# Optimization experiments

Measured on AMD Instinct MI355X. Metric: run time of the kernel, lower is better.

The kernel has to match this reference:

```python
import jax, jax.numpy as jnp
import numpy as np

N_NODES = 100000
N_EDGES = 1600000
D_IN = 256
D_OUT = 128


def setup_inputs() -> dict:
    key = jax.random.key(0)
    ks = jax.random.split(key, 7)
    h = jax.random.normal(ks[0], (N_NODES, D_IN), dtype=jnp.float32)
    src = jax.random.randint(ks[1], (N_EDGES,), 0, N_NODES, dtype=jnp.int32)
    dst = jax.random.randint(ks[2], (N_EDGES,), 0, N_NODES, dtype=jnp.int32)
    W = jax.random.normal(ks[3], (D_IN, D_OUT), dtype=jnp.float32) * (1.0 / np.sqrt(D_IN))
    b = jax.random.normal(ks[4], (D_OUT,), dtype=jnp.float32) * 0.01
    w_att = jax.random.normal(ks[5], (2 * D_OUT, 1), dtype=jnp.float32) * (1.0 / np.sqrt(2 * D_OUT))
    b_att = jax.random.normal(ks[6], (1,), dtype=jnp.float32) * 0.01
    return {"h": h, "src": src, "dst": dst, "W": W, "b": b, "w_att": w_att, "b_att": b_att}


def reference(h, src, dst, W, b, w_att, b_att):
    # node projection: graph.ndata['h'] = self.linear(h)
    hp = h @ W + b  # [N, D_OUT]
    n = hp.shape[0]
    d = hp.shape[1]
    # edge attention: leaky_relu(att_linear(cat[h_src, h_dst]))
    # cat([hs, hd]) @ w_att == hs @ w_att[:d] + hd @ w_att[d:]  (avoids [E, 2d] concat)
    wa_s = w_att[:d, 0]  # [D_OUT]
    wa_d = w_att[d:, 0]  # [D_OUT]
    e = hp[src] @ wa_s + hp[dst] @ wa_d + b_att[0]  # [E]
    e = jax.nn.leaky_relu(e)  # default negative_slope 0.01 matches F.leaky_relu
    # segment softmax over each destination node's incoming edges
    emax = jax.ops.segment_max(e, dst, num_segments=n)  # [N]
    ex = jnp.exp(e - emax[dst])  # [E]
    denom = jax.ops.segment_sum(ex, dst, num_segments=n)  # [N]
    # weighted scatter-sum of src features: sum_e alpha_e * h_src_e
    num = jax.ops.segment_sum(ex[:, None] * hp[src], dst, num_segments=n)  # [N, D_OUT]
    out = num / jnp.where(denom > 0, denom, 1.0)[:, None]  # zero-in-degree nodes -> 0
    return out
```

## Files before the change

### kernel.cpp

```cpp
#include <hip/hip_runtime.h>
#include <hip/hip_bf16.h>

#define D_IN 256
#define D_OUT 128
#define BNODES 64
#define BCAP 1536
#define EPB 8192
#define MAXNB 1600

typedef __attribute__((ext_vector_type(8))) short bf16x8;
typedef __attribute__((ext_vector_type(4))) float f32x4;
typedef __attribute__((ext_vector_type(2))) float f32x2;

__device__ __forceinline__ unsigned short f2bf(float f) {
    unsigned u = __float_as_uint(f);
    unsigned r = ((u >> 16) & 1u) + 0x7FFFu;
    return (unsigned short)((u + r) >> 16);
}
__device__ __forceinline__ unsigned pk2(float a, float b) {
    return (unsigned)f2bf(a) | ((unsigned)f2bf(b) << 16);
}
__device__ __forceinline__ bf16x8 pack8(float4 a, float4 b) {
    union { uint4 u; bf16x8 v; } r;
    r.u.x = pk2(a.x, a.y); r.u.y = pk2(a.z, a.w);
    r.u.z = pk2(b.x, b.y); r.u.w = pk2(b.z, b.w);
    return r.v;
}
__device__ __forceinline__ void gload_lds16(const void* g, void* l) {
    __builtin_amdgcn_global_load_lds(
        (const __attribute__((address_space(1))) void*)g,
        (__attribute__((address_space(3))) void*)l, 16, 0, 0);
}

__global__ __launch_bounds__(256) void init_bcursor_kernel(int* __restrict__ bcursor, int nb)
{
    int i = blockIdx.x * 256 + threadIdx.x;
    if (i < nb) bcursor[i] = i * BCAP;
}

__global__ __launch_bounds__(256) void prep_kernel(
    const float* __restrict__ W, unsigned short* __restrict__ WbT)
{
    int idx = blockIdx.x * 256 + threadIdx.x;
    int k = idx >> 7;
    int c = idx & 127;
    WbT[(size_t)c * 256 + k] = f2bf(W[idx]);
}

__global__ __launch_bounds__(512, 4) void gemm_mfma_kernel(
    const float* __restrict__ h, const unsigned short* __restrict__ WbT,
    const float* __restrict__ b, const float* __restrict__ w_att,
    unsigned short* __restrict__ hpb,
    float* __restrict__ alpha_s, float* __restrict__ alpha_d,
    int n, int nstrips)
{
    __shared__ char bT[65536];
    const int t = threadIdx.x;
    const int wv = t >> 6, lane = t & 63;
    const int fr = lane & 15, fq = lane >> 4;
    const int swz = (fr & 7) << 4;

    #pragma unroll
    for (int j = 0; j < 8; ++j) {
        int col0 = wv * 16 + j * 2;
        int col  = col0 + (lane >> 5);
        int seg  = lane & 31;
        const char* src = (const char*)WbT + col * 512 + ((seg * 16) ^ ((col & 7) << 4));
        gload_lds16(src, bT + col0 * 512);
    }
    __syncthreads();

    const int strip = blockIdx.x * 8 + wv;
    if (strip >= nstrips) return;
    const int r0 = strip * 32;

    const float* arow[2];
    #pragma unroll
    for (int m = 0; m < 2; ++m) {
        int rg = r0 + m * 16 + fr;
        if (rg >= n) rg = n - 1;
        arow[m] = h + (size_t)rg * D_IN + fq * 8;
    }

    f32x4 acc[2][8];
    #pragma unroll
    for (int m = 0; m < 2; ++m)
        #pragma unroll
        for (int nn = 0; nn < 8; ++nn) acc[m][nn] = (f32x4){0.f, 0.f, 0.f, 0.f};

    float4 bufA[2][2][2];
    #pragma unroll
    for (int m = 0; m < 2; ++m) {
        const float4* ap = (const float4*)arow[m];
        bufA[0][m][0] = ap[0]; bufA[0][m][1] = ap[1];
    }

    #pragma unroll
    for (int kk = 0; kk < 8; ++kk) {
        const int cur = kk & 1, nxt = cur ^ 1;
        if (kk < 7) {
            #pragma unroll
            for (int m = 0; m < 2; ++m) {
                const float4* ap = (const float4*)(arow[m] + (kk + 1) * 32);
                bufA[nxt][m][0] = ap[0]; bufA[nxt][m][1] = ap[1];
            }
        }
        bf16x8 af[2];
        #pragma unroll
        for (int m = 0; m < 2; ++m)
            af[m] = pack8(bufA[cur][m][0], bufA[cur][m][1]);

        const int x = kk * 64 + fq * 16;
        #pragma unroll
        for (int nn = 0; nn < 8; ++nn) {
            bf16x8 bfr = *(const bf16x8*)(bT + (nn * 16 + fr) * 512 + (x ^ swz));
            acc[0][nn] = __builtin_amdgcn_mfma_f32_16x16x32_bf16(af[0], bfr, acc[0][nn], 0, 0, 0);
            acc[1][nn] = __builtin_amdgcn_mfma_f32_16x16x32_bf16(af[1], bfr, acc[1][nn], 0, 0, 0);
        }
    }

    float bcol[8], was[8], wad[8];
    #pragma unroll
    for (int nn = 0; nn < 8; ++nn) {
        int j = nn * 16 + fr;
        bcol[nn] = b[j]; was[nn] = w_att[j]; wad[nn] = w_att[D_OUT + j];
    }
    #pragma unroll
    for (int m = 0; m < 2; ++m) {
        #pragma unroll
        for (int reg = 0; reg < 4; ++reg) {
            const int grow = r0 + m * 16 + fq * 4 + reg;
            const bool ok = grow < n;
            float ps = 0.f, pd = 0.f;
            #pragma unroll
            for (int nn = 0; nn < 8; ++nn) {
                float vv = acc[m][nn][reg] + bcol[nn];
                ps += vv * was[nn];
                pd += vv * wad[nn];
                if (ok) hpb[(size_t)grow * D_OUT + nn * 16 + fr] = f2bf(vv);
            }
            #pragma unroll
            for (int o = 1; o < 16; o <<= 1) {
                ps += __shfl_xor(ps, o);
                pd += __shfl_xor(pd, o);
            }
            if (fr == 0 && ok) { alpha_s[grow] = ps; alpha_d[grow] = pd; }
        }
    }
}

__global__ __launch_bounds__(1024) void bucket_scatter_kernel(
    const int* __restrict__ src, const int* __restrict__ dst,
    const float* __restrict__ alpha_s, const float* __restrict__ alpha_d,
    const float* __restrict__ b_att, int* __restrict__ bcursor,
    int2* __restrict__ ebuf, int ne, int nb)
{
    __shared__ int lhist[MAXNB];
    __shared__ int gbase[MAXNB];
    __shared__ int lcur[MAXNB];
    const int t = threadIdx.x;
    for (int i = t; i < nb; i += 1024) { lhist[i] = 0; lcur[i] = 0; }
    __syncthreads();
    const int base = blockIdx.x * EPB;
    #pragma unroll
    for (int j = 0; j < EPB / 1024; ++j) {
        int idx = base + j * 1024 + t;
        if (idx < ne) atomicAdd(&lhist[dst[idx] >> 6], 1);
    }
    __syncthreads();
    for (int i = t; i < nb; i += 1024) {
        int c = lhist[i];
        gbase[i] = c ? atomicAdd(&bcursor[i], c) : 0;
    }
    __syncthreads();
    const float ba = b_att[0];
    #pragma unroll
    for (int j = 0; j < EPB / 1024; ++j) {
        int idx = base + j * 1024 + t;
        if (idx < ne) {
            int s = src[idx], d = dst[idx];
            float ev = alpha_s[s] + alpha_d[d] + ba;
            ev = (ev >= 0.f) ? ev : 0.01f * ev;
            int bkt = d >> 6;
            int pos = gbase[bkt] + atomicAdd(&lcur[bkt], 1);
            if (pos < (bkt + 1) * BCAP)
                ebuf[pos] = make_int2(s | ((d & 63) << 17), __float_as_int(ev));
        }
    }
}

__device__ __forceinline__ void acc8(f32x2* acc2, uint4 uv, float w) {
    acc2[0].x += w * __uint_as_float(uv.x << 16);
    acc2[0].y += w * __uint_as_float(uv.x & 0xFFFF0000u);
    acc2[1].x += w * __uint_as_float(uv.y << 16);
    acc2[1].y += w * __uint_as_float(uv.y & 0xFFFF0000u);
    acc2[2].x += w * __uint_as_float(uv.z << 16);
    acc2[2].y += w * __uint_as_float(uv.z & 0xFFFF0000u);
    acc2[3].x += w * __uint_as_float(uv.w << 16);
    acc2[3].y += w * __uint_as_float(uv.w & 0xFFFF0000u);
}

__global__ __launch_bounds__(512) void aggregate_kernel(
    const unsigned short* __restrict__ hpb, const int2* __restrict__ ebuf,
    const int* __restrict__ bcursor, float* __restrict__ out, int n)
{
    __shared__ int2 srec[BCAP];
    __shared__ int lhist[BNODES], lstart[BNODES], lcur[BNODES];
    __shared__ float lmax[BNODES], lden[BNODES];
    const int t = threadIdx.x;
    const int bk = blockIdx.x;
    const int node0 = bk << 6;
    const int base = bk * BCAP;
    int cnt = bcursor[bk] - base;
    cnt = min(cnt, BCAP);

    if (t < BNODES) { lhist[t] = 0; lden[t] = 0.f; }
    __syncthreads();
    for (int i = t; i < cnt; i += 512)
        atomicAdd(&lhist[(ebuf[base + i].x >> 17) & 63], 1);
    __syncthreads();
    if (t < BNODES) {
        int c0 = lhist[t];
        int incl = c0;
        #pragma unroll
        for (int o = 1; o < 64; o <<= 1) {
            int v = __shfl_up(incl, o);
            if (t >= o) incl += v;
        }
        lstart[t] = incl - c0;
        lcur[t]   = incl - c0;
    }
    __syncthreads();
    for (int i = t; i < cnt; i += 512) {
        int2 r = ebuf[base + i];
        int pos = atomicAdd(&lcur[(r.x >> 17) & 63], 1);
        srec[pos] = r;
    }
    __syncthreads();

    const int wv = t >> 6, lane = t & 63;
    const int q = lane >> 4, dlane = lane & 15;
    const uint4* hp4 = (const uint4*)hpb;

    #pragma unroll
    for (int p = 0; p < 2; ++p) {
        const int nd = p * 32 + wv * 4 + q;
        const int off = lstart[nd], c = lhist[nd];
        float m = -INFINITY;
        for (int i = dlane; i < c; i += 16)
            m = fmaxf(m, __int_as_float(srec[off + i].y));
        #pragma unroll
        for (int o = 8; o; o >>= 1) m = fmaxf(m, __shfl_xor(m, o));
        if (dlane == 0) lmax[nd] = m;
    }
    __syncthreads();

    for (int i = t; i < cnt; i += 512) {
        int2 r = srec[i];
        int nd = (r.x >> 17) & 63;
        float w = __expf(__int_as_float(r.y) - lmax[nd]);
        srec[i].y = __float_as_int(w);
        atomicAdd(&lden[nd], w);
    }
    __syncthreads();

    #pragma unroll
    for (int p = 0; p < 2; ++p) {
        const int nd = p * 32 + wv * 4 + q;
        const int gnode = node0 + nd;
        const int off = lstart[nd], c = lhist[nd];

        f32x2 acc2[4];
        #pragma unroll
        for (int k = 0; k < 4; ++k) acc2[k] = (f32x2){0.f, 0.f};

        for (int t0 = 0; t0 < c; t0 += 4) {
            const int cm1 = c - 1;
            int2 r0 = srec[off + min(t0 + 0, cm1)];
            int2 r1 = srec[off + min(t0 + 1, cm1)];
            int2 r2 = srec[off + min(t0 + 2, cm1)];
            int2 r3 = srec[off + min(t0 + 3, cm1)];
            float w0 = __int_as_float(r0.y);
            float w1 = (t0 + 1 < c) ? __int_as_float(r1.y) : 0.f;
            float w2 = (t0 + 2 < c) ? __int_as_float(r2.y) : 0.f;
            float w3 = (t0 + 3 < c) ? __int_as_float(r3.y) : 0.f;
            uint4 u0 = hp4[(size_t)(r0.x & 0x1FFFF) * 16 + dlane];
            uint4 u1 = hp4[(size_t)(r1.x & 0x1FFFF) * 16 + dlane];
            uint4 u2 = hp4[(size_t)(r2.x & 0x1FFFF) * 16 + dlane];
            uint4 u3 = hp4[(size_t)(r3.x & 0x1FFFF) * 16 + dlane];
            acc8(acc2, u0, w0);
            acc8(acc2, u1, w1);
            acc8(acc2, u2, w2);
            acc8(acc2, u3, w3);
        }

        if (gnode < n) {
            float inv = (c > 0) ? 1.f / lden[nd] : 0.f;
            float4 o0 = { acc2[0].x*inv, acc2[0].y*inv, acc2[1].x*inv, acc2[1].y*inv };
            float4 o1 = { acc2[2].x*inv, acc2[2].y*inv, acc2[3].x*inv, acc2[3].y*inv };
            float4* op = (float4*)(out + (size_t)gnode * D_OUT) + 2 * dlane;
            op[0] = o0;
            op[1] = o1;
        }
    }
}

extern "C" void kernel_launch(void* const* d_in, const int* in_sizes, int n_in,
                              void* d_out, int out_size, void* d_ws, size_t ws_size,
                              hipStream_t stream)
{
    const float* h     = (const float*)d_in[0];
    const int*   src   = (const int*)  d_in[1];
    const int*   dst   = (const int*)  d_in[2];
    const float* W     = (const float*)d_in[3];
    const float* b     = (const float*)d_in[4];
    const float* w_att = (const float*)d_in[5];
    const float* b_att = (const float*)d_in[6];
    float* out = (float*)d_out;

    const int n  = in_sizes[0] / D_IN;
    const int ne = in_sizes[1];
    const int nb = (n + BNODES - 1) / BNODES;
    const int nstrips = (n + 31) / 32;

    unsigned short* hpb = (unsigned short*)d_ws;
    float* alpha_s = (float*)d_ws + (size_t)n * 64;
    float* alpha_d = alpha_s + n;
    int2*  ebuf    = (int2*)(alpha_d + n);
    int*   bcursor = (int*)(ebuf + (size_t)nb * BCAP);
    unsigned short* WbT = (unsigned short*)(bcursor + nb);

    init_bcursor_kernel<<<(nb + 255) / 256, 256, 0, stream>>>(bcursor, nb);
    prep_kernel<<<128, 256, 0, stream>>>(W, WbT);
    gemm_mfma_kernel<<<(nstrips + 7) / 8, 512, 0, stream>>>(
        h, WbT, b, w_att, hpb, alpha_s, alpha_d, n, nstrips);
    bucket_scatter_kernel<<<(ne + EPB - 1) / EPB, 1024, 0, stream>>>(
        src, dst, alpha_s, alpha_d, b_att, bcursor, ebuf, ne, nb);
    aggregate_kernel<<<nb, 512, 0, stream>>>(hpb, ebuf, bcursor, out, n);
}
```

Before: 138.9 us.

## Fuse init into prep, shrink GEMM strips, per-wave histograms, fuse softmax

Merges the bcursor init kernel into the W-transpose prep kernel to save a launch. Halves the GEMM strip height to 16 rows per wave, doubling the grid and lowering register pressure, at the cost of reloading the LDS B tile in more blocks. In aggregation, it replaces block-wide LDS atomics with per-wave histograms and a stable per-wave prefix. It also folds the max, exp and denominator passes into the per-node loop using shuffles, which removes two block barriers and the shared lmax/lden arrays.

```diff
diff --git a/kernel.cpp b/kernel.cpp
--- a/kernel.cpp
+++ b/kernel.cpp
@@ -32,19 +32,18 @@
         (__attribute__((address_space(3))) void*)l, 16, 0, 0);
 }
 
-__global__ __launch_bounds__(256) void init_bcursor_kernel(int* __restrict__ bcursor, int nb)
-{
-    int i = blockIdx.x * 256 + threadIdx.x;
-    if (i < nb) bcursor[i] = i * BCAP;
-}
-
 __global__ __launch_bounds__(256) void prep_kernel(
-    const float* __restrict__ W, unsigned short* __restrict__ WbT)
+    const float* __restrict__ W, unsigned short* __restrict__ WbT,
+    int* __restrict__ bcursor, int nb)
 {
     int idx = blockIdx.x * 256 + threadIdx.x;
-    int k = idx >> 7;
-    int c = idx & 127;
-    WbT[(size_t)c * 256 + k] = f2bf(W[idx]);
+    if (idx < 32768) {
+        int k = idx >> 7;
+        int c = idx & 127;
+        WbT[(size_t)c * 256 + k] = f2bf(W[idx]);
+    }
+    int j = idx - 32768;
+    if (j >= 0 && j < nb) bcursor[j] = j * BCAP;
 }
 
 __global__ __launch_bounds__(512, 4) void gemm_mfma_kernel(
@@ -72,51 +71,36 @@
 
     const int strip = blockIdx.x * 8 + wv;
     if (strip >= nstrips) return;
-    const int r0 = strip * 32;
-
-    const float* arow[2];
-    #pragma unroll
-    for (int m = 0; m < 2; ++m) {
-        int rg = r0 + m * 16 + fr;
-        if (rg >= n) rg = n - 1;
-        arow[m] = h + (size_t)rg * D_IN + fq * 8;
-    }
-
-    f32x4 acc[2][8];
-    #pragma unroll
-    for (int m = 0; m < 2; ++m)
-        #pragma unroll
-        for (int nn = 0; nn < 8; ++nn) acc[m][nn] = (f32x4){0.f, 0.f, 0.f, 0.f};
-
-    float4 bufA[2][2][2];
-    #pragma unroll
-    for (int m = 0; m < 2; ++m) {
-        const float4* ap = (const float4*)arow[m];
-        bufA[0][m][0] = ap[0]; bufA[0][m][1] = ap[1];
+    const int r0 = strip * 16;
+
+    int rg = r0 + fr;
+    if (rg >= n) rg = n - 1;
+    const float* arow = h + (size_t)rg * D_IN + fq * 8;
+
+    f32x4 acc[8];
+    #pragma unroll
+    for (int nn = 0; nn < 8; ++nn) acc[nn] = (f32x4){0.f, 0.f, 0.f, 0.f};
+
+    float4 a0, a1, na0, na1;
+    {
+        const float4* ap = (const float4*)arow;
+        a0 = ap[0]; a1 = ap[1];
     }
 
     #pragma unroll
     for (int kk = 0; kk < 8; ++kk) {
-        const int cur = kk & 1, nxt = cur ^ 1;
         if (kk < 7) {
-            #pragma unroll
-            for (int m = 0; m < 2; ++m) {
-                const float4* ap = (const float4*)(arow[m] + (kk + 1) * 32);
-                bufA[nxt][m][0] = ap[0]; bufA[nxt][m][1] = ap[1];
-            }
-        }
-        bf16x8 af[2];
-        #pragma unroll
-        for (int m = 0; m < 2; ++m)
-            af[m] = pack8(bufA[cur][m][0], bufA[cur][m][1]);
-
+            const float4* ap = (const float4*)(arow + (kk + 1) * 32);
+            na0 = ap[0]; na1 = ap[1];
+        }
+        bf16x8 af = pack8(a0, a1);
         const int x = kk * 64 + fq * 16;
         #pragma unroll
         for (int nn = 0; nn < 8; ++nn) {
             bf16x8 bfr = *(const bf16x8*)(bT + (nn * 16 + fr) * 512 + (x ^ swz));
-            acc[0][nn] = __builtin_amdgcn_mfma_f32_16x16x32_bf16(af[0], bfr, acc[0][nn], 0, 0, 0);
-            acc[1][nn] = __builtin_amdgcn_mfma_f32_16x16x32_bf16(af[1], bfr, acc[1][nn], 0, 0, 0);
-        }
+            acc[nn] = __builtin_amdgcn_mfma_f32_16x16x32_bf16(af, bfr, acc[nn], 0, 0, 0);
+        }
+        a0 = na0; a1 = na1;
     }
 
     float bcol[8], was[8], wad[8];
@@ -126,26 +110,23 @@
         bcol[nn] = b[j]; was[nn] = w_att[j]; wad[nn] = w_att[D_OUT + j];
     }
     #pragma unroll
-    for (int m = 0; m < 2; ++m) {
-        #pragma unroll
-        for (int reg = 0; reg < 4; ++reg) {
-            const int grow = r0 + m * 16 + fq * 4 + reg;
-            const bool ok = grow < n;
-            float ps = 0.f, pd = 0.f;
-            #pragma unroll
-            for (int nn = 0; nn < 8; ++nn) {
-                float vv = acc[m][nn][reg] + bcol[nn];
-                ps += vv * was[nn];
-                pd += vv * wad[nn];
-                if (ok) hpb[(size_t)grow * D_OUT + nn * 16 + fr] = f2bf(vv);
-            }
-            #pragma unroll
-            for (int o = 1; o < 16; o <<= 1) {
-                ps += __shfl_xor(ps, o);
-                pd += __shfl_xor(pd, o);
-            }
-            if (fr == 0 && ok) { alpha_s[grow] = ps; alpha_d[grow] = pd; }
-        }
+    for (int reg = 0; reg < 4; ++reg) {
+        const int grow = r0 + fq * 4 + reg;
+        const bool ok = grow < n;
+        float ps = 0.f, pd = 0.f;
+        #pragma unroll
+        for (int nn = 0; nn < 8; ++nn) {
+            float vv = acc[nn][reg] + bcol[nn];
+            ps += vv * was[nn];
+            pd += vv * wad[nn];
+            if (ok) hpb[(size_t)grow * D_OUT + nn * 16 + fr] = f2bf(vv);
+        }
+        #pragma unroll
+        for (int o = 1; o < 16; o <<= 1) {
+            ps += __shfl_xor(ps, o);
+            pd += __shfl_xor(pd, o);
+        }
+        if (fr == 0 && ok) { alpha_s[grow] = ps; alpha_d[grow] = pd; }
     }
 }
 
@@ -205,70 +186,78 @@
     const int* __restrict__ bcursor, float* __restrict__ out, int n)
 {
     __shared__ int2 srec[BCAP];
-    __shared__ int lhist[BNODES], lstart[BNODES], lcur[BNODES];
-    __shared__ float lmax[BNODES], lden[BNODES];
+    __shared__ int whist[8][BNODES];
+    __shared__ int lstart[BNODES], lhist[BNODES];
     const int t = threadIdx.x;
+    const int wv = t >> 6, lane = t & 63;
     const int bk = blockIdx.x;
     const int node0 = bk << 6;
     const int base = bk * BCAP;
     int cnt = bcursor[bk] - base;
     cnt = min(cnt, BCAP);
 
-    if (t < BNODES) { lhist[t] = 0; lden[t] = 0.f; }
-    __syncthreads();
-    for (int i = t; i < cnt; i += 512)
-        atomicAdd(&lhist[(ebuf[base + i].x >> 17) & 63], 1);
-    __syncthreads();
+    whist[wv][lane] = 0;
+    __syncthreads();
+
+    const int chunk = (cnt + 7) >> 3;
+    const int c0 = wv * chunk;
+    const int c1 = min(c0 + chunk, cnt);
+    for (int i = c0 + lane; i < c1; i += 64)
+        atomicAdd(&whist[wv][(ebuf[base + i].x >> 17) & 63], 1);
+    __syncthreads();
+
     if (t < BNODES) {
-        int c0 = lhist[t];
-        int incl = c0;
+        int tot = 0;
+        #pragma unroll
+        for (int w = 0; w < 8; ++w) tot += whist[w][t];
+        lhist[t] = tot;
+        int incl = tot;
         #pragma unroll
         for (int o = 1; o < 64; o <<= 1) {
             int v = __shfl_up(incl, o);
             if (t >= o) incl += v;
         }
-        lstart[t] = incl - c0;
-        lcur[t]   = incl - c0;
-    }
-    __syncthreads();
-    for (int i = t; i < cnt; i += 512) {
+        int run = incl - tot;
+        lstart[t] = run;
+        #pragma unroll
+        for (int w = 0; w < 8; ++w) {
+            int cw = whist[w][t];
+            whist[w][t] = run;
+            run += cw;
+        }
+    }
+    __syncthreads();
+
+    for (int i = c0 + lane; i < c1; i += 64) {
         int2 r = ebuf[base + i];
-        int pos = atomicAdd(&lcur[(r.x >> 17) & 63], 1);
+        int pos = atomicAdd(&whist[wv][(r.x >> 17) & 63], 1);
         srec[pos] = r;
     }
     __syncthreads();
 
-    const int wv = t >> 6, lane = t & 63;
     const int q = lane >> 4, dlane = lane & 15;
     const uint4* hp4 = (const uint4*)hpb;
-
-    #pragma unroll
-    for (int p = 0; p < 2; ++p) {
-        const int nd = p * 32 + wv * 4 + q;
-        const int off = lstart[nd], c = lhist[nd];
-        float m = -INFINITY;
-        for (int i = dlane; i < c; i += 16)
-            m = fmaxf(m, __int_as_float(srec[off + i].y));
-        #pragma unroll
-        for (int o = 8; o; o >>= 1) m = fmaxf(m, __shfl_xor(m, o));
-        if (dlane == 0) lmax[nd] = m;
-    }
-    __syncthreads();
-
-    for (int i = t; i < cnt; i += 512) {
-        int2 r = srec[i];
-        int nd = (r.x >> 17) & 63;
-        float w = __expf(__int_as_float(r.y) - lmax[nd]);
-        srec[i].y = __float_as_int(w);
-        atomicAdd(&lden[nd], w);
-    }
-    __syncthreads();
 
     #pragma unroll
     for (int p = 0; p < 2; ++p) {
         const int nd = p * 32 + wv * 4 + q;
         const int gnode = node0 + nd;
         const int off = lstart[nd], c = lhist[nd];
+
+        float m = -INFINITY;
+        for (int i = dlane; i < c; i += 16)
+            m = fmaxf(m, __int_as_float(srec[off + i].y));
+        #pragma unroll
+        for (int o = 8; o; o >>= 1) m = fmaxf(m, __shfl_xor(m, o));
+
+        float denom = 0.f;
+        for (int i = dlane; i < c; i += 16) {
+            float w = __expf(__int_as_float(srec[off + i].y) - m);
+            srec[off + i].y = __float_as_int(w);
+            denom += w;
+        }
+        #pragma unroll
+        for (int o = 8; o; o >>= 1) denom += __shfl_xor(denom, o);
 
         f32x2 acc2[4];
         #pragma unroll
@@ -295,7 +284,7 @@
         }
 
         if (gnode < n) {
-            float inv = (c > 0) ? 1.f / lden[nd] : 0.f;
+            float inv = (c > 0) ? 1.f / denom : 0.f;
             float4 o0 = { acc2[0].x*inv, acc2[0].y*inv, acc2[1].x*inv, acc2[1].y*inv };
             float4 o1 = { acc2[2].x*inv, acc2[2].y*inv, acc2[3].x*inv, acc2[3].y*inv };
             float4* op = (float4*)(out + (size_t)gnode * D_OUT) + 2 * dlane;
@@ -321,7 +310,7 @@
     const int n  = in_sizes[0] / D_IN;
     const int ne = in_sizes[1];
     const int nb = (n + BNODES - 1) / BNODES;
-    const int nstrips = (n + 31) / 32;
+    const int nstrips = (n + 15) / 16;
 
     unsigned short* hpb = (unsigned short*)d_ws;
     float* alpha_s = (float*)d_ws + (size_t)n * 64;
@@ -330,8 +319,7 @@
     int*   bcursor = (int*)(ebuf + (size_t)nb * BCAP);
     unsigned short* WbT = (unsigned short*)(bcursor + nb);
 
-    init_bcursor_kernel<<<(nb + 255) / 256, 256, 0, stream>>>(bcursor, nb);
-    prep_kernel<<<128, 256, 0, stream>>>(W, WbT);
+    prep_kernel<<<(32768 + nb + 255) / 256, 256, 0, stream>>>(W, WbT, bcursor, nb);
     gemm_mfma_kernel<<<(nstrips + 7) / 8, 512, 0, stream>>>(
         h, WbT, b, w_att, hpb, alpha_s, alpha_d, n, nstrips);
     bucket_scatter_kernel<<<(ne + EPB - 1) / EPB, 1024, 0, stream>>>(
```

Result: no change. 137.4 us (-1.1%).
